# Performance work log

Hardware: AMD Instinct MI355X
Metric: run time of the kernel (lower is better)

Reference implementation:

```python
import jax, jax.numpy as jnp
import numpy as np

N_NODES = 50000
N_EDGES = 600000
N_RELS = 16
N_GRAPHS = 128
IN_DIM = 128
REL_LAYERS = [128, 256, 128]
HIDDEN = [128, 256, 128]
N_CLASSES = 8


def setup_inputs() -> dict:
    key = jax.random.key(0)
    ks = jax.random.split(key, 24)
    inp = {}
    inp["h"] = jax.random.normal(ks[0], (N_NODES, IN_DIM), dtype=jnp.float32)
    inp["src"] = jax.random.randint(ks[1], (N_EDGES,), 0, N_NODES)
    inp["dst"] = jax.random.randint(ks[2], (N_EDGES,), 0, N_NODES)
    inp["rel_types"] = jax.random.randint(ks[3], (N_EDGES,), 0, N_RELS)
    inp["graph_ids"] = jnp.sort(jax.random.randint(ks[4], (N_NODES,), 0, N_GRAPHS))
    # RelGraphConv params per layer: W_rel [R,din,dout], W_loop [din,dout], b [dout]
    prev = IN_DIM
    ki = 5
    for i, d in enumerate(REL_LAYERS):
        inp[f"W_rel{i}"] = jax.random.normal(ks[ki], (N_RELS, prev, d), dtype=jnp.float32) * 0.05
        inp[f"W_loop{i}"] = jax.random.normal(ks[ki + 1], (prev, d), dtype=jnp.float32) * 0.05
        inp[f"b{i}"] = jnp.zeros((d,), dtype=jnp.float32)
        prev = d
        ki += 2
    for i, d in enumerate(HIDDEN):
        inp[f"Wh{i}"] = jax.random.normal(ks[ki], (prev, d), dtype=jnp.float32) * 0.05
        inp[f"bh{i}"] = jnp.zeros((d,), dtype=jnp.float32)
        prev = d
        ki += 1
    inp["Wc"] = jax.random.normal(ks[ki], (prev, N_CLASSES), dtype=jnp.float32) * 0.05
    inp["bc"] = jnp.zeros((N_CLASSES,), dtype=jnp.float32)
    return inp


def _rel_graph_conv(h, src, dst, rel, W_rel, W_loop, b):
    # transform every node under every relation: [R, N, dout]
    t = jnp.einsum("nd,rde->rne", h, W_rel)
    msgs = t[rel, src]  # [E, dout] gather per edge
    agg = jax.ops.segment_sum(msgs, dst, num_segments=h.shape[0])
    return jax.nn.relu(agg + h @ W_loop + b)  # self-loop + bias (DGL defaults)


def _forward(h, src, dst, rel_types, graph_ids,
             W_rel0, W_loop0, b0, W_rel1, W_loop1, b1, W_rel2, W_loop2, b2,
             Wh0, bh0, Wh1, bh1, Wh2, bh2, Wc, bc):
    h = h.astype(jnp.float32)
    for Wr, Wl, b in ((W_rel0, W_loop0, b0), (W_rel1, W_loop1, b1), (W_rel2, W_loop2, b2)):
        h = _rel_graph_conv(h, src, dst, rel_types, Wr, Wl, b)
    # dgl.mean_nodes: per-graph mean pooling
    sums = jax.ops.segment_sum(h, graph_ids, num_segments=N_GRAPHS)
    cnts = jax.ops.segment_sum(jnp.ones((h.shape[0],), h.dtype), graph_ids, num_segments=N_GRAPHS)
    hg = sums / jnp.maximum(cnts, 1.0)[:, None]
    for W, b in ((Wh0, bh0), (Wh1, bh1), (Wh2, bh2)):
        hg = jax.nn.relu(hg @ W + b)
    return jax.nn.softmax(hg @ Wc + bc, axis=1)


def reference(h, src, dst, rel_types, graph_ids,
              W_rel0, W_loop0, b0, W_rel1, W_loop1, b1, W_rel2, W_loop2, b2,
              Wh0, bh0, Wh1, bh1, Wh2, bh2, Wc, bc):
    return _forward(h, src, dst, rel_types, graph_ids,
                    W_rel0, W_loop0, b0, W_rel1, W_loop1, b1, W_rel2, W_loop2, b2,
                    Wh0, bh0, Wh1, bh1, Wh2, bh2, Wc, bc)
```

## Files before the change

kernel.cpp:

```cpp
#include <hip/hip_runtime.h>
#include <stdint.h>

#define NN 50000
#define NE 600000
#define NR 16
#define NG 128
#define TS 128
#define SCAN_B 512
#define NB_SCAN ((NN + SCAN_B - 1) / SCAN_B)
#define MAXB 1024

typedef short bf16x8 __attribute__((ext_vector_type(8)));
typedef float f32x4 __attribute__((ext_vector_type(4)));

static __device__ __forceinline__ unsigned short f2bf(float x) {
    unsigned int b = __float_as_uint(x);
    b += 0x7FFFu + ((b >> 16) & 1u);
    return (unsigned short)(b >> 16);
}
static __device__ __forceinline__ float bf2f(unsigned short u) {
    return __uint_as_float(((unsigned int)u) << 16);
}


__global__ void k_hist(const int* __restrict__ rel, const int* __restrict__ dst,
                       int* __restrict__ bcnt, int* __restrict__ ncnt, int npc, int B) {
    __shared__ int lh[MAXB];
    for (int i = threadIdx.x; i < B; i += 256) lh[i] = 0;
    __syncthreads();
    for (int e = blockIdx.x * blockDim.x + threadIdx.x; e < NE; e += gridDim.x * blockDim.x) {
        int d = dst[e];
        atomicAdd(&lh[(d / npc) * NR + rel[e]], 1);
        atomicAdd(&ncnt[d], 1);
    }
    __syncthreads();
    for (int i = threadIdx.x; i < B; i += 256) atomicAdd(&bcnt[i], lh[i]);
}

__global__ void k_scan1(const int* __restrict__ ncnt, int* __restrict__ bsum) {
    __shared__ int s[SCAN_B];
    int i = blockIdx.x * SCAN_B + threadIdx.x;
    s[threadIdx.x] = (i < NN) ? ncnt[i] : 0;
    __syncthreads();
    for (int off = SCAN_B / 2; off > 0; off >>= 1) {
        if (threadIdx.x < off) s[threadIdx.x] += s[threadIdx.x + off];
        __syncthreads();
    }
    if (threadIdx.x == 0) bsum[blockIdx.x] = s[0];
}

__global__ void k_scan2(const int* __restrict__ bsum, int* __restrict__ bpref, int* __restrict__ rowptr) {
    if (threadIdx.x == 0 && blockIdx.x == 0) {
        int run = 0;
        for (int b = 0; b < NB_SCAN; ++b) { bpref[b] = run; run += bsum[b]; }
        rowptr[NN] = run;
    }
}

__global__ void k_scan3(const int* __restrict__ ncnt, const int* __restrict__ bpref,
                        int* __restrict__ rowptr) {
    __shared__ int s[SCAN_B];
    int i = blockIdx.x * SCAN_B + threadIdx.x;
    int val = (i < NN) ? ncnt[i] : 0;
    s[threadIdx.x] = val;
    __syncthreads();
    for (int off = 1; off < SCAN_B; off <<= 1) {
        int x = (threadIdx.x >= off) ? s[threadIdx.x - off] : 0;
        __syncthreads();
        s[threadIdx.x] += x;
        __syncthreads();
    }
    if (i < NN) rowptr[i] = bpref[blockIdx.x] + s[threadIdx.x] - val;
}

__global__ __launch_bounds__(1024)
void k_scan_buckets(const int* __restrict__ bcnt, int B, int npc,
                    const int* __restrict__ rowptr,
                    int* __restrict__ boff, int* __restrict__ tstart,
                    int4* __restrict__ tilemap) {
    __shared__ int s1[MAXB], s2[MAXB];
    __shared__ int e_ex[MAXB + 1], t_ex[MAXB + 1];
    int tid = threadIdx.x;
    int v1 = (tid < B) ? bcnt[tid] : 0;
    int v2 = (v1 + TS - 1) / TS;
    s1[tid] = v1; s2[tid] = v2;
    __syncthreads();
    for (int off = 1; off < MAXB; off <<= 1) {
        int a1 = (tid >= off) ? s1[tid - off] : 0;
        int a2 = (tid >= off) ? s2[tid - off] : 0;
        __syncthreads();
        s1[tid] += a1; s2[tid] += a2;
        __syncthreads();
    }
    if (tid < B) {
        e_ex[tid] = s1[tid] - v1;
        t_ex[tid] = s2[tid] - v2;
        boff[tid] = e_ex[tid];
        tstart[tid] = t_ex[tid];
        if (tid == B - 1) {
            e_ex[B] = s1[tid]; t_ex[B] = s2[tid];
            boff[B] = s1[tid]; tstart[B] = s2[tid];
        }
    }
    __syncthreads();
    int T = t_ex[B];
    for (int t = tid; t < T; t += 1024) {
        int lo = 0, hi = B - 1;
        while (lo < hi) {
            int mid = (lo + hi + 1) >> 1;
            if (t_ex[mid] <= t) lo = mid; else hi = mid - 1;
        }
        int b = lo;
        int tt = t - t_ex[b];
        int v1b = e_ex[b + 1] - e_ex[b];
        int rem = v1b - tt * TS;
        int cnt = rem < TS ? rem : TS;
        int chunk = b >> 4;
        int nstart = chunk * npc; if (nstart > NN) nstart = NN;
        tilemap[t] = make_int4(b & (NR - 1), e_ex[b] + tt * TS, cnt, rowptr[nstart]);
    }
}

__global__ void k_scatter(const int* __restrict__ rel, const int* __restrict__ dst,
                          const int* __restrict__ src,
                          const int* __restrict__ boff, int* __restrict__ cursor,
                          const int* __restrict__ rowptr, int* __restrict__ ncur,
                          int* __restrict__ srcs, int* __restrict__ dpos, int npc, int B) {
    __shared__ int lh[MAXB];
    const int CH = 4096;
    int e0 = blockIdx.x * CH;
    for (int i = threadIdx.x; i < B; i += 256) lh[i] = 0;
    __syncthreads();
    for (int i = threadIdx.x; i < CH; i += 256) {
        int e = e0 + i;
        if (e < NE) atomicAdd(&lh[(dst[e] / npc) * NR + rel[e]], 1);
    }
    __syncthreads();
    for (int i = threadIdx.x; i < B; i += 256) {
        int c = lh[i];
        lh[i] = (c > 0) ? atomicAdd(&cursor[i], c) : 0;
    }
    __syncthreads();
    for (int i = threadIdx.x; i < CH; i += 256) {
        int e = e0 + i;
        if (e < NE) {
            int d = dst[e];
            int b = (d / npc) * NR + rel[e];
            int p = boff[b] + atomicAdd(&lh[b], 1);
            int pd = rowptr[d] + atomicAdd(&ncur[d], 1);
            srcs[p] = src[e];
            dpos[p] = pd;
        }
    }
}


__global__ void k_hconv(const float* __restrict__ h, unsigned short* __restrict__ hb, int n4) {
    int i = blockIdx.x * 256 + threadIdx.x;
    if (i < n4) {
        float4 v = reinterpret_cast<const float4*>(h)[i];
        ushort4 o = { f2bf(v.x), f2bf(v.y), f2bf(v.z), f2bf(v.w) };
        reinterpret_cast<ushort4*>(hb)[i] = o;
    }
}

__global__ void k_wconv_all(const float* Wr0, const float* Wr1, const float* Wr2,
                            const float* Wl0, const float* Wl1, const float* Wl2,
                            unsigned short* Wt0, unsigned short* Wt1, unsigned short* Wt2,
                            unsigned short* Wlt0, unsigned short* Wlt1, unsigned short* Wlt2) {
    const float* W; unsigned short* O; int R, Kd, Nd;
    switch (blockIdx.y) {
        case 0:  W = Wr0; O = Wt0;  R = NR; Kd = 128; Nd = 128; break;
        case 1:  W = Wr1; O = Wt1;  R = NR; Kd = 128; Nd = 256; break;
        case 2:  W = Wr2; O = Wt2;  R = NR; Kd = 256; Nd = 128; break;
        case 3:  W = Wl0; O = Wlt0; R = 1;  Kd = 128; Nd = 128; break;
        case 4:  W = Wl1; O = Wlt1; R = 1;  Kd = 128; Nd = 256; break;
        default: W = Wl2; O = Wlt2; R = 1;  Kd = 256; Nd = 128; break;
    }
    int total = R * Kd * Nd;
    for (int i = blockIdx.x * 256 + threadIdx.x; i < total; i += gridDim.x * 256) {
        int r = i / (Kd * Nd);
        int rem = i - r * Kd * Nd;
        int k = rem / Nd;
        int n = rem - k * Nd;
        O[((size_t)r * Nd + n) * Kd + k] = f2bf(W[i]);
    }
}


template<int K>
__global__ __launch_bounds__(256, 4)
void k_dense_mfma(const unsigned short* __restrict__ hb,
                  const unsigned short* __restrict__ Wlt,
                  const float* __restrict__ bias,
                  float* __restrict__ outbuf, int ldn) {
    __shared__ __align__(16) unsigned short As[128][72];
    __shared__ __align__(16) unsigned short Bs[128][72];
    const int tid = threadIdx.x;
    const int row0 = blockIdx.x * 128;
    const int colbase = blockIdx.y * 128;
    const int lane = tid & 63, w = tid >> 6;
    const int quad = lane >> 4, col = lane & 15;
    const int srow = tid >> 3, sk = (tid & 7) * 8;

    f32x4 acc[8][2];
#pragma unroll
    for (int i = 0; i < 8; ++i) { acc[i][0] = 0.f; acc[i][1] = 0.f; }

    for (int k0 = 0; k0 < K; k0 += 64) {
        __syncthreads();
#pragma unroll
        for (int pp = 0; pp < 4; ++pp) {
            int rw = pp * 32 + srow;
            int ar = row0 + rw; if (ar >= NN) ar = NN - 1;
            *reinterpret_cast<uint4*>(&As[rw][sk]) =
                *reinterpret_cast<const uint4*>(hb + (size_t)ar * K + k0 + sk);
            *reinterpret_cast<uint4*>(&Bs[rw][sk]) =
                *reinterpret_cast<const uint4*>(Wlt + (size_t)(colbase + rw) * K + k0 + sk);
        }
        __syncthreads();
#pragma unroll
        for (int s = 0; s < 2; ++s) {
            bf16x8 bf0 = *reinterpret_cast<const bf16x8*>(&Bs[w * 32 + col][s * 32 + quad * 8]);
            bf16x8 bf1 = *reinterpret_cast<const bf16x8*>(&Bs[w * 32 + 16 + col][s * 32 + quad * 8]);
#pragma unroll
            for (int rt = 0; rt < 8; ++rt) {
                bf16x8 af = *reinterpret_cast<const bf16x8*>(&As[rt * 16 + col][s * 32 + quad * 8]);
                acc[rt][0] = __builtin_amdgcn_mfma_f32_16x16x32_bf16(af, bf0, acc[rt][0], 0, 0, 0);
                acc[rt][1] = __builtin_amdgcn_mfma_f32_16x16x32_bf16(af, bf1, acc[rt][1], 0, 0, 0);
            }
        }
    }
    float bv0 = bias[colbase + w * 32 + col];
    float bv1 = bias[colbase + w * 32 + 16 + col];
#pragma unroll
    for (int rt = 0; rt < 8; ++rt) {
#pragma unroll
        for (int reg = 0; reg < 4; ++reg) {
            int r = row0 + rt * 16 + quad * 4 + reg;
            if (r < NN) {
                float* dp = outbuf + (size_t)r * ldn + colbase + w * 32;
                dp[col] = acc[rt][0][reg] + bv0;
                dp[16 + col] = acc[rt][1][reg] + bv1;
            }
        }
    }
}


template<int K>
__global__ __launch_bounds__(256, 4)
void k_edge_mfma(const unsigned short* __restrict__ hb,
                 const unsigned short* __restrict__ Wt,
                 int ldn, int colbase,
                 const int* __restrict__ srcs, const int* __restrict__ dpos,
                 const int4* __restrict__ tilemap, const int* __restrict__ tstart,
                 int chunkBase,
                 unsigned short* __restrict__ msg, int capRows) {
    const int tb0 = tstart[chunkBase];
    const int tend = tstart[chunkBase + NR];
    const int t = tb0 + blockIdx.x;
    if (t >= tend) return;
    const int4 tm = tilemap[t];
    const int r = tm.x, e0 = tm.y, cnt = tm.z, cES = tm.w;

    __shared__ __align__(16) unsigned short As[128][132];
    __shared__ int s_src[TS], s_out[TS];
    const int tid = threadIdx.x;
    if (tid < TS) {
        int ei = e0 + (tid < cnt ? tid : cnt - 1);
        s_src[tid] = srcs[ei];
        int row = dpos[ei] - cES;
        s_out[tid] = (tid < cnt && row < capRows) ? row : -1;
    }
    __syncthreads();

    const unsigned short* Wb = Wt + ((size_t)r * ldn + colbase) * K;
    const int lane = tid & 63, w = tid >> 6;
    const int quad = lane >> 4, col = lane & 15;
    const int asr = tid >> 4, ask = (tid & 15) * 8;

    f32x4 acc[8][2];
#pragma unroll
    for (int i = 0; i < 8; ++i) { acc[i][0] = 0.f; acc[i][1] = 0.f; }

    for (int kk = 0; kk < K; kk += 128) {
        if (kk) __syncthreads();
#pragma unroll
        for (int q = 0; q < 8; ++q) {
            int rw = q * 16 + asr;
            *reinterpret_cast<uint4*>(&As[rw][ask]) =
                *reinterpret_cast<const uint4*>(hb + (size_t)s_src[rw] * K + kk + ask);
        }
        __syncthreads();
#pragma unroll
        for (int k32 = 0; k32 < 4; ++k32) {
            bf16x8 bf0 = *reinterpret_cast<const bf16x8*>(
                Wb + (size_t)(w * 32 + col) * K + kk + k32 * 32 + quad * 8);
            bf16x8 bf1 = *reinterpret_cast<const bf16x8*>(
                Wb + (size_t)(w * 32 + 16 + col) * K + kk + k32 * 32 + quad * 8);
#pragma unroll
            for (int rt = 0; rt < 8; ++rt) {
                bf16x8 af = *reinterpret_cast<const bf16x8*>(&As[rt * 16 + col][k32 * 32 + quad * 8]);
                acc[rt][0] = __builtin_amdgcn_mfma_f32_16x16x32_bf16(af, bf0, acc[rt][0], 0, 0, 0);
                acc[rt][1] = __builtin_amdgcn_mfma_f32_16x16x32_bf16(af, bf1, acc[rt][1], 0, 0, 0);
            }
        }
    }
#pragma unroll
    for (int rt = 0; rt < 8; ++rt) {
#pragma unroll
        for (int reg = 0; reg < 4; ++reg) {
            int m = rt * 16 + quad * 4 + reg;
            int o = s_out[m];
            if (o >= 0) {
                unsigned short* dp = msg + (size_t)o * 128 + w * 32;
                dp[col] = f2bf(acc[rt][0][reg]);
                dp[16 + col] = f2bf(acc[rt][1][reg]);
            }
        }
    }
}

__global__ __launch_bounds__(256)
void k_reduce(const unsigned short* __restrict__ msg,
              const float* __restrict__ selfb, int ld_self, int co_self,
              unsigned short* __restrict__ out_bf, int ld_bf, int co_bf,
              float* __restrict__ out_f32, int ld_f32, int co_f32,
              const int* __restrict__ rowptr, int n0, int npc, int capRows) {
    int idx = blockIdx.x * 4 + (threadIdx.x >> 6);
    int n = n0 + idx;
    if (idx >= npc || n >= NN) return;
    int lane = threadIdx.x & 63;
    int cES = rowptr[n0];
    float2 acc = *reinterpret_cast<const float2*>(selfb + (size_t)n * ld_self + co_self + lane * 2);
    int j0 = rowptr[n], j1 = rowptr[n + 1];
    int jcap = cES + capRows; if (j1 > jcap) j1 = jcap;
    const unsigned int* mp = reinterpret_cast<const unsigned int*>(msg) + lane;
    int j = j0;
    for (; j + 4 <= j1; j += 4) {
        unsigned int m0 = mp[(size_t)(j + 0 - cES) * 64];
        unsigned int m1 = mp[(size_t)(j + 1 - cES) * 64];
        unsigned int m2 = mp[(size_t)(j + 2 - cES) * 64];
        unsigned int m3 = mp[(size_t)(j + 3 - cES) * 64];
        acc.x += bf2f((unsigned short)(m0 & 0xffffu)) + bf2f((unsigned short)(m1 & 0xffffu))
               + bf2f((unsigned short)(m2 & 0xffffu)) + bf2f((unsigned short)(m3 & 0xffffu));
        acc.y += bf2f((unsigned short)(m0 >> 16)) + bf2f((unsigned short)(m1 >> 16))
               + bf2f((unsigned short)(m2 >> 16)) + bf2f((unsigned short)(m3 >> 16));
    }
    for (; j < j1; ++j) {
        unsigned int m = mp[(size_t)(j - cES) * 64];
        acc.x += bf2f((unsigned short)(m & 0xffffu));
        acc.y += bf2f((unsigned short)(m >> 16));
    }
    acc.x = acc.x > 0.f ? acc.x : 0.f;
    acc.y = acc.y > 0.f ? acc.y : 0.f;
    if (out_bf) {
        unsigned int o = (unsigned int)f2bf(acc.x) | ((unsigned int)f2bf(acc.y) << 16);
        *reinterpret_cast<unsigned int*>(out_bf + (size_t)n * ld_bf + co_bf + lane * 2) = o;
    }
    if (out_f32) {
        *reinterpret_cast<float2*>(out_f32 + (size_t)n * ld_f32 + co_f32 + lane * 2) = acc;
    }
}


__global__ void k_pool(const float* __restrict__ h, const int* __restrict__ gid,
                       float* __restrict__ hg, float* __restrict__ gcnt) {
    const int c = threadIdx.x;
    int n0 = blockIdx.x * 64;
    if (n0 >= NN) return;
    int end = n0 + 64; if (end > NN) end = NN;
    int cur = gid[n0];
    float run = 0.f, crun = 0.f;
    for (int n = n0; n < end; ++n) {
        int g = gid[n];
        if (g != cur) {
            atomicAdd(&hg[cur * 128 + c], run);
            if (c == 0) atomicAdd(&gcnt[cur], crun);
            run = 0.f; crun = 0.f; cur = g;
        }
        run += h[(size_t)n * 128 + c];
        crun += 1.f;
    }
    atomicAdd(&hg[cur * 128 + c], run);
    if (c == 0) atomicAdd(&gcnt[cur], crun);
}

__global__ __launch_bounds__(256)
void k_head(const float* __restrict__ hg, const float* __restrict__ gcnt,
            const float* __restrict__ Wh0, const float* __restrict__ bh0,
            const float* __restrict__ Wh1, const float* __restrict__ bh1,
            const float* __restrict__ Wh2, const float* __restrict__ bh2,
            const float* __restrict__ Wc, const float* __restrict__ bc,
            float* __restrict__ out) {
    __shared__ float x0[128], x1[128], x2[256], x3[128], sl[8];
    int g = blockIdx.x, t = threadIdx.x;
    if (t < 128) {
        float c = gcnt[g];
        x0[t] = hg[g * 128 + t] / (c > 1.f ? c : 1.f);
    }
    __syncthreads();
    if (t < 128) {
        float a = bh0[t];
        for (int k = 0; k < 128; ++k) a += x0[k] * Wh0[k * 128 + t];
        x1[t] = a > 0.f ? a : 0.f;
    }
    __syncthreads();
    {
        float a = bh1[t];
        for (int k = 0; k < 128; ++k) a += x1[k] * Wh1[k * 256 + t];
        x2[t] = a > 0.f ? a : 0.f;
    }
    __syncthreads();
    if (t < 128) {
        float a = bh2[t];
        for (int k = 0; k < 256; ++k) a += x2[k] * Wh2[k * 128 + t];
        x3[t] = a > 0.f ? a : 0.f;
    }
    __syncthreads();
    if (t < 8) {
        float a = bc[t];
        for (int k = 0; k < 128; ++k) a += x3[k] * Wc[k * 8 + t];
        sl[t] = a;
    }
    __syncthreads();
    if (t == 0) {
        float m = sl[0];
        for (int c = 1; c < 8; ++c) m = sl[c] > m ? sl[c] : m;
        float s = 0.f, e[8];
        for (int c = 0; c < 8; ++c) { e[c] = expf(sl[c] - m); s += e[c]; }
        for (int c = 0; c < 8; ++c) out[g * 8 + c] = e[c] / s;
    }
}


extern "C" void kernel_launch(void* const* d_in, const int* in_sizes, int n_in,
                              void* d_out, int out_size, void* d_ws, size_t ws_size,
                              hipStream_t stream) {
    const float* h0   = (const float*)d_in[0];
    const int* src    = (const int*)d_in[1];
    const int* dst    = (const int*)d_in[2];
    const int* rel    = (const int*)d_in[3];
    const int* gid    = (const int*)d_in[4];
    const float* Wr0  = (const float*)d_in[5];
    const float* Wl0  = (const float*)d_in[6];
    const float* b0   = (const float*)d_in[7];
    const float* Wr1  = (const float*)d_in[8];
    const float* Wl1  = (const float*)d_in[9];
    const float* b1   = (const float*)d_in[10];
    const float* Wr2  = (const float*)d_in[11];
    const float* Wl2  = (const float*)d_in[12];
    const float* b2   = (const float*)d_in[13];
    const float* Wh0  = (const float*)d_in[14];
    const float* bh0  = (const float*)d_in[15];
    const float* Wh1  = (const float*)d_in[16];
    const float* bh1  = (const float*)d_in[17];
    const float* Wh2  = (const float*)d_in[18];
    const float* bh2  = (const float*)d_in[19];
    const float* Wc   = (const float*)d_in[20];
    const float* bc   = (const float*)d_in[21];
    float* out = (float*)d_out;

    char* p = (char*)d_ws;
    auto alloc = [&](size_t bytes) { char* q = p; p += (bytes + 255) & ~(size_t)255; return q; };
    float* bufS  = (float*)alloc((size_t)NN * 256 * 4);
    unsigned short* hbA = (unsigned short*)alloc((size_t)NN * 256 * 2);
    unsigned short* hbB = (unsigned short*)alloc((size_t)NN * 128 * 2);
    unsigned short* Wt0 = (unsigned short*)alloc((size_t)NR * 128 * 128 * 2);
    unsigned short* Wt1 = (unsigned short*)alloc((size_t)NR * 256 * 128 * 2);
    unsigned short* Wt2 = (unsigned short*)alloc((size_t)NR * 128 * 256 * 2);
    unsigned short* Wlt0 = (unsigned short*)alloc((size_t)128 * 128 * 2);
    unsigned short* Wlt1 = (unsigned short*)alloc((size_t)256 * 128 * 2);
    unsigned short* Wlt2 = (unsigned short*)alloc((size_t)128 * 256 * 2);
    int* srcs    = (int*)alloc((size_t)NE * 4);
    int* dpos    = (int*)alloc((size_t)NE * 4);
    int* rowptr  = (int*)alloc((size_t)(NN + 1) * 4);
    int* bsum    = (int*)alloc(NB_SCAN * 4);
    int* bpref   = (int*)alloc(NB_SCAN * 4);
    int* boff    = (int*)alloc((MAXB + 1) * 4);
    int* tstart  = (int*)alloc((MAXB + 1) * 4);
    int4* tilemap = (int4*)alloc((size_t)(NE / TS + MAXB + 64) * 16);
    char* zbase  = p;
    int* bcnt    = (int*)alloc(MAXB * 4);
    int* cursor  = (int*)alloc(MAXB * 4);
    int* ncnt    = (int*)alloc((size_t)NN * 4);
    int* ncur    = (int*)alloc((size_t)NN * 4);
    float* hg    = (float*)alloc((size_t)NG * 128 * 4);
    float* gcnt  = (float*)alloc(NG * 4);
    size_t zlen  = (size_t)(p - zbase);
    unsigned short* msg = (unsigned short*)p;

    long long avail = (long long)ws_size - (long long)(p - (char*)d_ws);
    if (avail < (1 << 20)) avail = (1 << 20);
    long long capR64 = avail / 256;
    int C = 64;
    for (int c = 1; c <= 64; ++c) {
        double need = (double)NE / c * 1.15 + 4096.0;
        if ((double)capR64 >= need) { C = c; break; }
    }
    int npc = (NN + C - 1) / C;
    int B = C * NR;
    int capRows = capR64 > 2000000000LL ? 2000000000 : (int)capR64;
    int TPC = (int)((double)NE / C * 1.15 / TS) + NR + 8;
    int RDB = (npc + 3) / 4;

    hipMemsetAsync(zbase, 0, zlen, stream);
    k_hist<<<256, 256, 0, stream>>>(rel, dst, bcnt, ncnt, npc, B);
    k_scan1<<<NB_SCAN, SCAN_B, 0, stream>>>(ncnt, bsum);
    k_scan2<<<1, 64, 0, stream>>>(bsum, bpref, rowptr);
    k_scan3<<<NB_SCAN, SCAN_B, 0, stream>>>(ncnt, bpref, rowptr);
    k_scan_buckets<<<1, MAXB, 0, stream>>>(bcnt, B, npc, rowptr, boff, tstart, tilemap);
    k_scatter<<<(NE + 4095) / 4096, 256, 0, stream>>>(rel, dst, src, boff, cursor, rowptr, ncur, srcs, dpos, npc, B);

    k_hconv<<<(NN * 128 / 4 + 255) / 256, 256, 0, stream>>>(h0, hbA, NN * 128 / 4);
    k_wconv_all<<<dim3(512, 6), 256, 0, stream>>>(Wr0, Wr1, Wr2, Wl0, Wl1, Wl2,
                                                  Wt0, Wt1, Wt2, Wlt0, Wlt1, Wlt2);

    const int RB = (NN + TS - 1) / TS;

    k_dense_mfma<128><<<dim3(RB, 1), 256, 0, stream>>>(hbA, Wlt0, b0, bufS, 128);
    for (int c = 0; c < C; ++c) {
        k_edge_mfma<128><<<TPC, 256, 0, stream>>>(hbA, Wt0, 128, 0, srcs, dpos, tilemap, tstart, c * NR, msg, capRows);
        k_reduce<<<RDB, 256, 0, stream>>>(msg, bufS, 128, 0, hbB, 128, 0, (float*)nullptr, 0, 0, rowptr, c * npc, npc, capRows);
    }

    k_dense_mfma<128><<<dim3(RB, 2), 256, 0, stream>>>(hbB, Wlt1, b1, bufS, 256);
    for (int half = 0; half < 2; ++half) {
        for (int c = 0; c < C; ++c) {
            k_edge_mfma<128><<<TPC, 256, 0, stream>>>(hbB, Wt1, 256, half * 128, srcs, dpos, tilemap, tstart, c * NR, msg, capRows);
            k_reduce<<<RDB, 256, 0, stream>>>(msg, bufS, 256, half * 128, hbA, 256, half * 128, (float*)nullptr, 0, 0, rowptr, c * npc, npc, capRows);
        }
    }

    k_dense_mfma<256><<<dim3(RB, 1), 256, 0, stream>>>(hbA, Wlt2, b2, bufS, 128);
    for (int c = 0; c < C; ++c) {
        k_edge_mfma<256><<<TPC, 256, 0, stream>>>(hbA, Wt2, 128, 0, srcs, dpos, tilemap, tstart, c * NR, msg, capRows);
        k_reduce<<<RDB, 256, 0, stream>>>(msg, bufS, 128, 0, (unsigned short*)nullptr, 0, 0, bufS, 128, 0, rowptr, c * npc, npc, capRows);
    }

    k_pool<<<(NN + 63) / 64, 128, 0, stream>>>(bufS, gid, hg, gcnt);
    k_head<<<NG, 256, 0, stream>>>(hg, gcnt, Wh0, bh0, Wh1, bh1, Wh2, bh2, Wc, bc, out);
}
```

Before: 748.4 us.

## Sub-bucket edges by source-node range to improve gather locality

Edge buckets are now keyed by destination chunk, source-node stripe and relation instead of destination chunk and relation only. The stripe count S is chosen so the total bucket count fills MAXB. Within each destination chunk, edge tiles then gather from a narrower source-row range, which should improve cache hit rates for the h gathers. It also changes the LDS row padding from 132 to 136. The cost is more partially filled tiles, since there are more buckets per chunk, and a larger launch grid per chunk.

```diff
diff --git a/kernel.cpp b/kernel.cpp
--- a/kernel.cpp
+++ b/kernel.cpp
@@ -24,13 +24,16 @@
 
 
 __global__ void k_hist(const int* __restrict__ rel, const int* __restrict__ dst,
-                       int* __restrict__ bcnt, int* __restrict__ ncnt, int npc, int B) {
+                       const int* __restrict__ src,
+                       int* __restrict__ bcnt, int* __restrict__ ncnt,
+                       int npc, int nps, int SB, int B) {
     __shared__ int lh[MAXB];
     for (int i = threadIdx.x; i < B; i += 256) lh[i] = 0;
     __syncthreads();
     for (int e = blockIdx.x * blockDim.x + threadIdx.x; e < NE; e += gridDim.x * blockDim.x) {
         int d = dst[e];
-        atomicAdd(&lh[(d / npc) * NR + rel[e]], 1);
+        int key = (d / npc) * SB + (src[e] / nps) * NR + rel[e];
+        atomicAdd(&lh[key], 1);
         atomicAdd(&ncnt[d], 1);
     }
     __syncthreads();
@@ -74,7 +77,7 @@
 }
 
 __global__ __launch_bounds__(1024)
-void k_scan_buckets(const int* __restrict__ bcnt, int B, int npc,
+void k_scan_buckets(const int* __restrict__ bcnt, int B, int npc, int SB,
                     const int* __restrict__ rowptr,
                     int* __restrict__ boff, int* __restrict__ tstart,
                     int4* __restrict__ tilemap) {
@@ -115,7 +118,7 @@
         int v1b = e_ex[b + 1] - e_ex[b];
         int rem = v1b - tt * TS;
         int cnt = rem < TS ? rem : TS;
-        int chunk = b >> 4;
+        int chunk = b / SB;
         int nstart = chunk * npc; if (nstart > NN) nstart = NN;
         tilemap[t] = make_int4(b & (NR - 1), e_ex[b] + tt * TS, cnt, rowptr[nstart]);
     }
@@ -125,7 +128,8 @@
                           const int* __restrict__ src,
                           const int* __restrict__ boff, int* __restrict__ cursor,
                           const int* __restrict__ rowptr, int* __restrict__ ncur,
-                          int* __restrict__ srcs, int* __restrict__ dpos, int npc, int B) {
+                          int* __restrict__ srcs, int* __restrict__ dpos,
+                          int npc, int nps, int SB, int B) {
     __shared__ int lh[MAXB];
     const int CH = 4096;
     int e0 = blockIdx.x * CH;
@@ -133,7 +137,7 @@
     __syncthreads();
     for (int i = threadIdx.x; i < CH; i += 256) {
         int e = e0 + i;
-        if (e < NE) atomicAdd(&lh[(dst[e] / npc) * NR + rel[e]], 1);
+        if (e < NE) atomicAdd(&lh[(dst[e] / npc) * SB + (src[e] / nps) * NR + rel[e]], 1);
     }
     __syncthreads();
     for (int i = threadIdx.x; i < B; i += 256) {
@@ -145,10 +149,11 @@
         int e = e0 + i;
         if (e < NE) {
             int d = dst[e];
-            int b = (d / npc) * NR + rel[e];
+            int s = src[e];
+            int b = (d / npc) * SB + (s / nps) * NR + rel[e];
             int p = boff[b] + atomicAdd(&lh[b], 1);
             int pd = rowptr[d] + atomicAdd(&ncur[d], 1);
-            srcs[p] = src[e];
+            srcs[p] = s;
             dpos[p] = pd;
         }
     }
@@ -255,16 +260,16 @@
                  int ldn, int colbase,
                  const int* __restrict__ srcs, const int* __restrict__ dpos,
                  const int4* __restrict__ tilemap, const int* __restrict__ tstart,
-                 int chunkBase,
+                 int chunkBase, int SB,
                  unsigned short* __restrict__ msg, int capRows) {
     const int tb0 = tstart[chunkBase];
-    const int tend = tstart[chunkBase + NR];
+    const int tend = tstart[chunkBase + SB];
     const int t = tb0 + blockIdx.x;
     if (t >= tend) return;
     const int4 tm = tilemap[t];
     const int r = tm.x, e0 = tm.y, cnt = tm.z, cES = tm.w;
 
-    __shared__ __align__(16) unsigned short As[128][132];
+    __shared__ __align__(16) unsigned short As[128][136];
     __shared__ int s_src[TS], s_out[TS];
     const int tid = threadIdx.x;
     if (tid < TS) {
@@ -500,18 +505,21 @@
         if ((double)capR64 >= need) { C = c; break; }
     }
     int npc = (NN + C - 1) / C;
-    int B = C * NR;
+    int S = MAXB / (C * NR); if (S < 1) S = 1;
+    int SB = S * NR;
+    int B = C * SB;
+    int nps = (NN + S - 1) / S;
     int capRows = capR64 > 2000000000LL ? 2000000000 : (int)capR64;
-    int TPC = (int)((double)NE / C * 1.15 / TS) + NR + 8;
+    int TPC = (int)((double)NE / C * 1.15 / TS) + SB + 8;
     int RDB = (npc + 3) / 4;
 
     hipMemsetAsync(zbase, 0, zlen, stream);
-    k_hist<<<256, 256, 0, stream>>>(rel, dst, bcnt, ncnt, npc, B);
+    k_hist<<<256, 256, 0, stream>>>(rel, dst, src, bcnt, ncnt, npc, nps, SB, B);
     k_scan1<<<NB_SCAN, SCAN_B, 0, stream>>>(ncnt, bsum);
     k_scan2<<<1, 64, 0, stream>>>(bsum, bpref, rowptr);
     k_scan3<<<NB_SCAN, SCAN_B, 0, stream>>>(ncnt, bpref, rowptr);
-    k_scan_buckets<<<1, MAXB, 0, stream>>>(bcnt, B, npc, rowptr, boff, tstart, tilemap);
-    k_scatter<<<(NE + 4095) / 4096, 256, 0, stream>>>(rel, dst, src, boff, cursor, rowptr, ncur, srcs, dpos, npc, B);
+    k_scan_buckets<<<1, MAXB, 0, stream>>>(bcnt, B, npc, SB, rowptr, boff, tstart, tilemap);
+    k_scatter<<<(NE + 4095) / 4096, 256, 0, stream>>>(rel, dst, src, boff, cursor, rowptr, ncur, srcs, dpos, npc, nps, SB, B);
 
     k_hconv<<<(NN * 128 / 4 + 255) / 256, 256, 0, stream>>>(h0, hbA, NN * 128 / 4);
     k_wconv_all<<<dim3(512, 6), 256, 0, stream>>>(Wr0, Wr1, Wr2, Wl0, Wl1, Wl2,
@@ -521,21 +529,21 @@
 
     k_dense_mfma<128><<<dim3(RB, 1), 256, 0, stream>>>(hbA, Wlt0, b0, bufS, 128);
     for (int c = 0; c < C; ++c) {
-        k_edge_mfma<128><<<TPC, 256, 0, stream>>>(hbA, Wt0, 128, 0, srcs, dpos, tilemap, tstart, c * NR, msg, capRows);
+        k_edge_mfma<128><<<TPC, 256, 0, stream>>>(hbA, Wt0, 128, 0, srcs, dpos, tilemap, tstart, c * SB, SB, msg, capRows);
         k_reduce<<<RDB, 256, 0, stream>>>(msg, bufS, 128, 0, hbB, 128, 0, (float*)nullptr, 0, 0, rowptr, c * npc, npc, capRows);
     }
 
     k_dense_mfma<128><<<dim3(RB, 2), 256, 0, stream>>>(hbB, Wlt1, b1, bufS, 256);
     for (int half = 0; half < 2; ++half) {
         for (int c = 0; c < C; ++c) {
-            k_edge_mfma<128><<<TPC, 256, 0, stream>>>(hbB, Wt1, 256, half * 128, srcs, dpos, tilemap, tstart, c * NR, msg, capRows);
+            k_edge_mfma<128><<<TPC, 256, 0, stream>>>(hbB, Wt1, 256, half * 128, srcs, dpos, tilemap, tstart, c * SB, SB, msg, capRows);
             k_reduce<<<RDB, 256, 0, stream>>>(msg, bufS, 256, half * 128, hbA, 256, half * 128, (float*)nullptr, 0, 0, rowptr, c * npc, npc, capRows);
         }
     }
 
     k_dense_mfma<256><<<dim3(RB, 1), 256, 0, stream>>>(hbA, Wlt2, b2, bufS, 128);
     for (int c = 0; c < C; ++c) {
-        k_edge_mfma<256><<<TPC, 256, 0, stream>>>(hbA, Wt2, 128, 0, srcs, dpos, tilemap, tstart, c * NR, msg, capRows);
+        k_edge_mfma<256><<<TPC, 256, 0, stream>>>(hbA, Wt2, 128, 0, srcs, dpos, tilemap, tstart, c * SB, SB, msg, capRows);
         k_reduce<<<RDB, 256, 0, stream>>>(msg, bufS, 128, 0, (unsigned short*)nullptr, 0, 0, bufS, 128, 0, rowptr, c * npc, npc, capRows);
     }
 
```

After: 747.4 us. Within noise of the previous version (-0.1%).
